# Performance work log

Hardware: AMD Instinct MI355X
Metric: run time of the kernel (lower is better)

Reference implementation:

```python
import jax, jax.numpy as jnp
import numpy as np

N = 50000   # vertices
E = 25000   # hyperedges
NNZ = 400000  # incidence pairs (v, e)
D_IN = 512
D_OUT = 512  # heads * out_channels, heads=1


def setup_inputs() -> dict:
    key = jax.random.key(0)
    kx, kw, kv, ke = jax.random.split(key, 4)
    X = jax.random.normal(kx, (N, D_IN), dtype=jnp.float32)
    W = jax.random.normal(kw, (D_OUT, D_IN), dtype=jnp.float32) * 0.02  # nn.Linear weight [out,in]
    vidx = jax.random.randint(kv, (NNZ,), 0, N, dtype=jnp.int32)
    eidx = jax.random.randint(ke, (NNZ,), 0, E, dtype=jnp.int32)
    # degE = 1/|e| (hyperedge size), degV = 1/deg(v), as precomputed by hyperg
    ones = jnp.ones((NNZ,), dtype=jnp.float32)
    edge_sz = jax.ops.segment_sum(ones, eidx, num_segments=E)
    vert_dg = jax.ops.segment_sum(ones, vidx, num_segments=N)
    degE = 1.0 / jnp.maximum(edge_sz, 1.0)
    degV = 1.0 / jnp.maximum(vert_dg, 1.0)
    Wdiag = jnp.ones((E,), dtype=jnp.float32)
    return {"X": X, "W": W, "degE": degE, "degV": degV, "Wdiag": Wdiag,
            "vidx": vidx, "eidx": eidx}


def reference(X, W, degE, degV, Wdiag, vidx, eidx):
    # Dense projection: X @ W^T (nn.Linear, no bias)
    Xp = jnp.einsum('nd,od->no', X, W)                      # [N, D_OUT]
    # Stage 1: vertex -> hyperedge (first_aggr: mean via degE), weighted by Wdiag
    Xe = jax.ops.segment_sum(Xp[vidx], eidx, num_segments=E)  # [E, D_OUT]
    Xe = Xe * (degE * Wdiag)[:, None]
    # Stage 2: hyperedge -> vertex, normalized by degV
    Xv = jax.ops.segment_sum(Xe[eidx], vidx, num_segments=N)  # [N, D_OUT]
    Xv = Xv * degV[:, None]
    return Xv
```

## Files before the change

kernel.cpp:

```cpp
#include <hip/hip_runtime.h>

typedef unsigned short u16;
typedef unsigned int   u32;
typedef __attribute__((ext_vector_type(4))) float f32x4;
typedef __attribute__((ext_vector_type(4))) u32   u32x4;
typedef __attribute__((ext_vector_type(8))) __bf16 bf16x8;

constexpr int NV   = 50000;
constexpr int NE   = 25000;
constexpr int NNZp = 400000;
constexpr int D    = 512;
constexpr int MP   = 50048;
constexpr int NBE  = 25;
constexpr int NBV  = 49;

static __device__ __forceinline__ u16 f2bf(float f) {
  u32 u = __float_as_uint(f);
  u32 r = (u + 0x7fffu + ((u >> 16) & 1u)) >> 16;
  return (u16)r;
}
static __device__ __forceinline__ u32 pk2(float a, float b) {
  return (u32)f2bf(a) | ((u32)f2bf(b) << 16);
}

static __device__ __forceinline__ void gload_lds16(const u16* g, u16* l) {
  __builtin_amdgcn_global_load_lds(
      (const __attribute__((address_space(1))) u32*)g,
      (__attribute__((address_space(3))) u32*)l, 16, 0, 0);
}

__global__ void zero_kernel(int* cntE, int* cntV) {
  int i = blockIdx.x * 256 + threadIdx.x;
  if (i < NE) cntE[i] = 0;
  if (i < NV) cntV[i] = 0;
}

__global__ void hist_kernel(const int* __restrict__ vidx, const int* __restrict__ eidx,
                            int* cntE, int* cntV) {
  int i = blockIdx.x * 256 + threadIdx.x;
  if (i < NNZp) {
    atomicAdd(&cntE[eidx[i]], 1);
    atomicAdd(&cntV[vidx[i]], 1);
  }
}

__global__ __launch_bounds__(256) void scan1_kernel(
    const int* __restrict__ cntE, const int* __restrict__ cntV,
    int* offE, int* offV, int* blkSum) {
  const bool isE = blockIdx.x < NBE;
  const int* cnt = isE ? cntE : cntV;
  int* off = isE ? offE : offV;
  const int len = isE ? NE : NV;
  const int t = threadIdx.x;
  const int base = (isE ? blockIdx.x : blockIdx.x - NBE) * 1024 + t * 4;
  int4 c = {0, 0, 0, 0};
  if (base + 4 <= len) c = *(const int4*)(cnt + base);
  else {
    if (base + 0 < len) c.x = cnt[base + 0];
    if (base + 1 < len) c.y = cnt[base + 1];
    if (base + 2 < len) c.z = cnt[base + 2];
    if (base + 3 < len) c.w = cnt[base + 3];
  }
  int s = c.x + c.y + c.z + c.w;
  __shared__ int sm[256];
  sm[t] = s;
  __syncthreads();
  for (int d = 1; d < 256; d <<= 1) {
    int u = (t >= d) ? sm[t - d] : 0;
    __syncthreads();
    sm[t] += u;
    __syncthreads();
  }
  int ex = sm[t] - s;
  int4 o;
  o.x = ex; o.y = o.x + c.x; o.z = o.y + c.y; o.w = o.z + c.z;
  if (base + 4 <= len) *(int4*)(off + base) = o;
  else {
    if (base + 0 < len) off[base + 0] = o.x;
    if (base + 1 < len) off[base + 1] = o.y;
    if (base + 2 < len) off[base + 2] = o.z;
    if (base + 3 < len) off[base + 3] = o.w;
  }
  if (t == 255) blkSum[blockIdx.x] = sm[255];
}

__global__ void scan2_kernel(int* blkSum) {
  int wv = threadIdx.x >> 6, lane = threadIdx.x & 63;
  int off = wv ? NBE : 0, len = wv ? NBV : NBE;
  int v = (lane < len) ? blkSum[off + lane] : 0;
  int incl = v;
#pragma unroll
  for (int d = 1; d < 64; d <<= 1) {
    int u = __shfl_up(incl, d, 64);
    if (lane >= d) incl += u;
  }
  if (lane < len) blkSum[off + lane] = incl - v;
}

__global__ __launch_bounds__(256) void scan3_kernel(
    int* offE, int* offV, int* curE, int* curV, const int* __restrict__ blkSum) {
  const bool isE = blockIdx.x < NBE;
  int* off = isE ? offE : offV;
  int* cur = isE ? curE : curV;
  const int len = isE ? NE : NV;
  const int pref = blkSum[blockIdx.x];
  const int base = (isE ? blockIdx.x : blockIdx.x - NBE) * 1024 + threadIdx.x * 4;
  if (base + 4 <= len) {
    int4 o = *(int4*)(off + base);
    o.x += pref; o.y += pref; o.z += pref; o.w += pref;
    *(int4*)(off + base) = o;
    *(int4*)(cur + base) = o;
  } else {
    for (int q = 0; q < 4; q++)
      if (base + q < len) { int v = off[base + q] + pref; off[base + q] = v; cur[base + q] = v; }
  }
}

__global__ void scatter_kernel(const int* __restrict__ vidx, const int* __restrict__ eidx,
                               int* curE, int* curV, int* csr_ev, int* csr_ve) {
  int i = blockIdx.x * 256 + threadIdx.x;
  if (i < NNZp) {
    int e = eidx[i], v = vidx[i];
    csr_ev[atomicAdd(&curE[e], 1)] = v;
    csr_ve[atomicAdd(&curV[v], 1)] = e;
  }
}

__global__ __launch_bounds__(256) void convert_kernel(
    const float* __restrict__ X, const float* __restrict__ W,
    u16* __restrict__ Xb, u16* __restrict__ Wb) {
  constexpr size_t NX = (size_t)NV * D;
  size_t i = ((size_t)blockIdx.x * 256 + threadIdx.x) * 8;
  const float* src;
  u16* dst;
  if (i < NX) { src = X + i; dst = Xb + i; }
  else        { src = W + (i - NX); dst = Wb + (i - NX); }
  f32x4 a = *(const f32x4*)src;
  f32x4 b = *(const f32x4*)(src + 4);
  u32x4 p = { pk2(a[0], a[1]), pk2(a[2], a[3]), pk2(b[0], b[1]), pk2(b[2], b[3]) };
  *(u32x4*)dst = p;
}

__global__ __launch_bounds__(256) void gemm_kernel(const u16* __restrict__ A,
                                                   const u16* __restrict__ B,
                                                   u16* __restrict__ C) {
  __shared__ u16 sA[128 * 32];
  __shared__ u16 sB[128 * 32];
  const int tid  = threadIdx.x;
  const int lane = tid & 63;
  const int wave = tid >> 6;
  const int bm = blockIdx.y * 128;
  const int bn = blockIdx.x * 128;
  const int wm = (wave >> 1) * 64;
  const int wn = (wave & 1) * 64;
  const int lr = lane & 15;
  const int lk = (lane >> 4) * 8;
  const int srow = lane >> 2;
  const int scol = (lane & 3) * 8;

  f32x4 acc[4][4] = {};

  for (int kt = 0; kt < D; kt += 32) {
    __syncthreads();
#pragma unroll
    for (int c = 0; c < 2; c++) {
      const int ar = wave * 16 + c * 64;
      gload_lds16(A + (size_t)(bm + ar + srow) * D + kt + scol, &sA[ar * 32]);
      gload_lds16(B + (size_t)(bn + ar + srow) * D + kt + scol, &sB[ar * 32]);
    }
    __syncthreads();

    bf16x8 af[4], bfr[4];
#pragma unroll
    for (int i = 0; i < 4; i++) af[i]  = *(const bf16x8*)&sA[(wm + i * 16 + lr) * 32 + lk];
#pragma unroll
    for (int j = 0; j < 4; j++) bfr[j] = *(const bf16x8*)&sB[(wn + j * 16 + lr) * 32 + lk];
#pragma unroll
    for (int i = 0; i < 4; i++)
#pragma unroll
      for (int j = 0; j < 4; j++)
        acc[i][j] = __builtin_amdgcn_mfma_f32_16x16x32_bf16(af[i], bfr[j], acc[i][j], 0, 0, 0);
  }

#pragma unroll
  for (int i = 0; i < 4; i++)
#pragma unroll
    for (int r = 0; r < 4; r++) {
      int row = bm + wm + i * 16 + (lane >> 4) * 4 + r;
      u16* crow = C + (size_t)row * D + bn + wn + lr;
#pragma unroll
      for (int j = 0; j < 4; j++) crow[j * 16] = f2bf(acc[i][j][r]);
    }
}

__global__ __launch_bounds__(256) void stage1_kernel(
    const u16* __restrict__ Xp, const int* __restrict__ offE, const int* __restrict__ cntE,
    const int* __restrict__ csr_ev, const float* __restrict__ degE,
    const float* __restrict__ Wdiag, u16* __restrict__ Xe) {
  const int lane = threadIdx.x & 63;
  const int e = blockIdx.x * 4 + (threadIdx.x >> 6);
  const int start = offE[e], cnt = cntE[e];
  float acc[8] = {};
  for (int base = 0; base < cnt; base += 64) {
    int n = min(64, cnt - base);
    int myidx = (base + lane < cnt) ? csr_ev[start + base + lane] : 0;
#pragma unroll 4
    for (int k = 0; k < n; k++) {
      int v = __shfl(myidx, k, 64);
      u32x4 p = *(const u32x4*)(Xp + (size_t)v * D + lane * 8);
#pragma unroll
      for (int q = 0; q < 4; q++) {
        u32 u = p[q];
        acc[2 * q]     += __uint_as_float(u << 16);
        acc[2 * q + 1] += __uint_as_float(u & 0xffff0000u);
      }
    }
  }
  float s = degE[e] * Wdiag[e];
  u32x4 o = { pk2(acc[0] * s, acc[1] * s), pk2(acc[2] * s, acc[3] * s),
              pk2(acc[4] * s, acc[5] * s), pk2(acc[6] * s, acc[7] * s) };
  *(u32x4*)(Xe + (size_t)e * D + lane * 8) = o;
}

__global__ __launch_bounds__(256) void stage2_kernel(
    const u16* __restrict__ Xe, const int* __restrict__ offV, const int* __restrict__ cntV,
    const int* __restrict__ csr_ve, const float* __restrict__ degV, float* __restrict__ out) {
  const int lane = threadIdx.x & 63;
  const int v = blockIdx.x * 4 + (threadIdx.x >> 6);
  const int start = offV[v], cnt = cntV[v];
  float acc[8] = {};
  for (int base = 0; base < cnt; base += 64) {
    int n = min(64, cnt - base);
    int myidx = (base + lane < cnt) ? csr_ve[start + base + lane] : 0;
#pragma unroll 4
    for (int k = 0; k < n; k++) {
      int e = __shfl(myidx, k, 64);
      u32x4 p = *(const u32x4*)(Xe + (size_t)e * D + lane * 8);
#pragma unroll
      for (int q = 0; q < 4; q++) {
        u32 u = p[q];
        acc[2 * q]     += __uint_as_float(u << 16);
        acc[2 * q + 1] += __uint_as_float(u & 0xffff0000u);
      }
    }
  }
  float s = degV[v];
  float* orow = out + (size_t)v * D + lane * 8;
  f32x4 o0 = { acc[0] * s, acc[1] * s, acc[2] * s, acc[3] * s };
  f32x4 o1 = { acc[4] * s, acc[5] * s, acc[6] * s, acc[7] * s };
  *(f32x4*)orow = o0;
  *(f32x4*)(orow + 4) = o1;
}

extern "C" void kernel_launch(void* const* d_in, const int* in_sizes, int n_in,
                              void* d_out, int out_size, void* d_ws, size_t ws_size,
                              hipStream_t stream) {
  const float* X     = (const float*)d_in[0];
  const float* W     = (const float*)d_in[1];
  const float* degE  = (const float*)d_in[2];
  const float* degV  = (const float*)d_in[3];
  const float* Wdiag = (const float*)d_in[4];
  const int*   vidx  = (const int*)d_in[5];
  const int*   eidx  = (const int*)d_in[6];
  float* out = (float*)d_out;

  char* p = (char*)d_ws;
  auto take = [&](size_t bytes) { char* r = p; p += (bytes + 255) & ~(size_t)255; return r; };
  u16* Xb     = (u16*)take((size_t)MP * D * 2);
  u16* Wb     = (u16*)take((size_t)D * D * 2);
  u16* Xp     = (u16*)take((size_t)MP * D * 2);
  u16* Xe     = (u16*)take((size_t)NE * D * 2);
  int* cntE   = (int*)take((size_t)NE * 4);
  int* offE   = (int*)take((size_t)NE * 4);
  int* curE   = (int*)take((size_t)NE * 4);
  int* cntV   = (int*)take((size_t)NV * 4);
  int* offV   = (int*)take((size_t)NV * 4);
  int* curV   = (int*)take((size_t)NV * 4);
  int* csr_ev = (int*)take((size_t)NNZp * 4);
  int* csr_ve = (int*)take((size_t)NNZp * 4);
  int* blkSum = (int*)take((size_t)(NBE + NBV) * 4);

  constexpr size_t NCONV = ((size_t)NV * D + (size_t)D * D) / 8 / 256;

  zero_kernel   <<<(NV + 255) / 256, 256, 0, stream>>>(cntE, cntV);
  hist_kernel   <<<(NNZp + 255) / 256, 256, 0, stream>>>(vidx, eidx, cntE, cntV);
  scan1_kernel  <<<NBE + NBV, 256, 0, stream>>>(cntE, cntV, offE, offV, blkSum);
  scan2_kernel  <<<1, 128, 0, stream>>>(blkSum);
  scan3_kernel  <<<NBE + NBV, 256, 0, stream>>>(offE, offV, curE, curV, blkSum);
  scatter_kernel<<<(NNZp + 255) / 256, 256, 0, stream>>>(vidx, eidx, curE, curV, csr_ev, csr_ve);
  convert_kernel<<<NCONV, 256, 0, stream>>>(X, W, Xb, Wb);
  gemm_kernel   <<<dim3(D / 128, MP / 128), 256, 0, stream>>>(Xb, Wb, Xp);
  stage1_kernel <<<NE / 4, 256, 0, stream>>>(Xp, offE, cntE, csr_ev, degE, Wdiag, Xe);
  stage2_kernel <<<NV / 4, 256, 0, stream>>>(Xe, offV, cntV, csr_ve, degV, out);
}
```

Before: 441.6 us.

## Split gather-reduce rows into column slices with 8 neighbors per wave in parallel

```diff
diff --git a/kernel.cpp b/kernel.cpp
--- a/kernel.cpp
+++ b/kernel.cpp
@@ -197,17 +197,20 @@
     const u16* __restrict__ Xp, const int* __restrict__ offE, const int* __restrict__ cntE,
     const int* __restrict__ csr_ev, const float* __restrict__ degE,
     const float* __restrict__ Wdiag, u16* __restrict__ Xe) {
-  const int lane = threadIdx.x & 63;
-  const int e = blockIdx.x * 4 + (threadIdx.x >> 6);
+  const int wave  = threadIdx.x >> 6;
+  const int lane  = threadIdx.x & 63;
+  const int g     = lane >> 3;
+  const int c     = lane & 7;
+  const int slice = blockIdx.x & 7;
+  const int e     = (blockIdx.x >> 3) * 4 + wave;
   const int start = offE[e], cnt = cntE[e];
+  const int col0  = slice * 64 + c * 8;
   float acc[8] = {};
-  for (int base = 0; base < cnt; base += 64) {
-    int n = min(64, cnt - base);
-    int myidx = (base + lane < cnt) ? csr_ev[start + base + lane] : 0;
-#pragma unroll 4
-    for (int k = 0; k < n; k++) {
-      int v = __shfl(myidx, k, 64);
-      u32x4 p = *(const u32x4*)(Xp + (size_t)v * D + lane * 8);
+  for (int base = 0; base < cnt; base += 8) {
+    int j = base + g;
+    if (j < cnt) {
+      int v = csr_ev[start + j];
+      u32x4 p = *(const u32x4*)(Xp + (size_t)v * D + col0);
 #pragma unroll
       for (int q = 0; q < 4; q++) {
         u32 u = p[q];
@@ -216,26 +219,39 @@
       }
     }
   }
-  float s = degE[e] * Wdiag[e];
-  u32x4 o = { pk2(acc[0] * s, acc[1] * s), pk2(acc[2] * s, acc[3] * s),
-              pk2(acc[4] * s, acc[5] * s), pk2(acc[6] * s, acc[7] * s) };
-  *(u32x4*)(Xe + (size_t)e * D + lane * 8) = o;
+#pragma unroll
+  for (int q = 0; q < 8; q++) {
+    float s = acc[q];
+    s += __shfl_xor(s, 8, 64);
+    s += __shfl_xor(s, 16, 64);
+    s += __shfl_xor(s, 32, 64);
+    acc[q] = s;
+  }
+  if (g == 0) {
+    float s = degE[e] * Wdiag[e];
+    u32x4 o = { pk2(acc[0] * s, acc[1] * s), pk2(acc[2] * s, acc[3] * s),
+                pk2(acc[4] * s, acc[5] * s), pk2(acc[6] * s, acc[7] * s) };
+    *(u32x4*)(Xe + (size_t)e * D + col0) = o;
+  }
 }
 
 __global__ __launch_bounds__(256) void stage2_kernel(
     const u16* __restrict__ Xe, const int* __restrict__ offV, const int* __restrict__ cntV,
     const int* __restrict__ csr_ve, const float* __restrict__ degV, float* __restrict__ out) {
-  const int lane = threadIdx.x & 63;
-  const int v = blockIdx.x * 4 + (threadIdx.x >> 6);
+  const int wave  = threadIdx.x >> 6;
+  const int lane  = threadIdx.x & 63;
+  const int g     = lane >> 3;
+  const int c     = lane & 7;
+  const int slice = blockIdx.x & 7;
+  const int v     = (blockIdx.x >> 3) * 4 + wave;
   const int start = offV[v], cnt = cntV[v];
+  const int col0  = slice * 64 + c * 8;
   float acc[8] = {};
-  for (int base = 0; base < cnt; base += 64) {
-    int n = min(64, cnt - base);
-    int myidx = (base + lane < cnt) ? csr_ve[start + base + lane] : 0;
-#pragma unroll 4
-    for (int k = 0; k < n; k++) {
-      int e = __shfl(myidx, k, 64);
-      u32x4 p = *(const u32x4*)(Xe + (size_t)e * D + lane * 8);
+  for (int base = 0; base < cnt; base += 8) {
+    int j = base + g;
+    if (j < cnt) {
+      int e = csr_ve[start + j];
+      u32x4 p = *(const u32x4*)(Xe + (size_t)e * D + col0);
 #pragma unroll
       for (int q = 0; q < 4; q++) {
         u32 u = p[q];
@@ -244,12 +260,22 @@
       }
     }
   }
-  float s = degV[v];
-  float* orow = out + (size_t)v * D + lane * 8;
-  f32x4 o0 = { acc[0] * s, acc[1] * s, acc[2] * s, acc[3] * s };
-  f32x4 o1 = { acc[4] * s, acc[5] * s, acc[6] * s, acc[7] * s };
-  *(f32x4*)orow = o0;
-  *(f32x4*)(orow + 4) = o1;
+#pragma unroll
+  for (int q = 0; q < 8; q++) {
+    float s = acc[q];
+    s += __shfl_xor(s, 8, 64);
+    s += __shfl_xor(s, 16, 64);
+    s += __shfl_xor(s, 32, 64);
+    acc[q] = s;
+  }
+  if (g == 0) {
+    float s = degV[v];
+    float* orow = out + (size_t)v * D + col0;
+    f32x4 o0 = { acc[0] * s, acc[1] * s, acc[2] * s, acc[3] * s };
+    f32x4 o1 = { acc[4] * s, acc[5] * s, acc[6] * s, acc[7] * s };
+    *(f32x4*)orow = o0;
+    *(f32x4*)(orow + 4) = o1;
+  }
 }
 
 extern "C" void kernel_launch(void* const* d_in, const int* in_sizes, int n_in,
@@ -290,6 +316,6 @@
   scatter_kernel<<<(NNZp + 255) / 256, 256, 0, stream>>>(vidx, eidx, curE, curV, csr_ev, csr_ve);
   convert_kernel<<<NCONV, 256, 0, stream>>>(X, W, Xb, Wb);
   gemm_kernel   <<<dim3(D / 128, MP / 128), 256, 0, stream>>>(Xb, Wb, Xp);
-  stage1_kernel <<<NE / 4, 256, 0, stream>>>(Xp, offE, cntE, csr_ev, degE, Wdiag, Xe);
-  stage2_kernel <<<NV / 4, 256, 0, stream>>>(Xe, offV, cntV, csr_ve, degV, out);
-}
+  stage1_kernel <<<(NE / 4) * 8, 256, 0, stream>>>(Xp, offE, cntE, csr_ev, degE, Wdiag, Xe);
+  stage2_kernel <<<(NV / 4) * 8, 256, 0, stream>>>(Xe, offV, cntV, csr_ve, degV, out);
+}
```

New measurement: 538.9 us. 22.1% more time.

## Split gather-aggregation columns into XCD-mapped slices for L2 locality

Applied to the files above, without the earlier changes.

```diff
diff --git a/kernel.cpp b/kernel.cpp
--- a/kernel.cpp
+++ b/kernel.cpp
@@ -13,6 +13,8 @@
 constexpr int MP   = 50048;
 constexpr int NBE  = 25;
 constexpr int NBV  = 49;
+constexpr int SG1  = 391;
+constexpr int SG2  = 1563;
 
 static __device__ __forceinline__ u16 f2bf(float f) {
   u32 u = __float_as_uint(f);
@@ -197,59 +199,75 @@
     const u16* __restrict__ Xp, const int* __restrict__ offE, const int* __restrict__ cntE,
     const int* __restrict__ csr_ev, const float* __restrict__ degE,
     const float* __restrict__ Wdiag, u16* __restrict__ Xe) {
+  const int wave = threadIdx.x >> 6;
   const int lane = threadIdx.x & 63;
-  const int e = blockIdx.x * 4 + (threadIdx.x >> 6);
-  const int start = offE[e], cnt = cntE[e];
+  const int g    = lane >> 2;
+  const int c    = lane & 3;
+  const int bid  = blockIdx.x;
+  const int xcd  = bid & 7;
+  const int tmp  = bid >> 3;
+  const int phase = (tmp >= SG1) ? 1 : 0;
+  const int sg    = tmp - phase * SG1;
+  const int slice = xcd + 8 * phase;
+  const int e     = sg * 64 + wave * 16 + g;
+  const int col0  = slice * 32 + c * 8;
+  int start = 0, cnt = 0;
+  if (e < NE) { start = offE[e]; cnt = cntE[e]; }
   float acc[8] = {};
-  for (int base = 0; base < cnt; base += 64) {
-    int n = min(64, cnt - base);
-    int myidx = (base + lane < cnt) ? csr_ev[start + base + lane] : 0;
-#pragma unroll 4
-    for (int k = 0; k < n; k++) {
-      int v = __shfl(myidx, k, 64);
-      u32x4 p = *(const u32x4*)(Xp + (size_t)v * D + lane * 8);
-#pragma unroll
-      for (int q = 0; q < 4; q++) {
-        u32 u = p[q];
-        acc[2 * q]     += __uint_as_float(u << 16);
-        acc[2 * q + 1] += __uint_as_float(u & 0xffff0000u);
-      }
+  int nxt = (cnt > 0) ? csr_ev[start] : 0;
+  for (int j = 0; j < cnt; j++) {
+    int v = nxt;
+    if (j + 1 < cnt) nxt = csr_ev[start + j + 1];
+    u32x4 p = *(const u32x4*)(Xp + (size_t)v * D + col0);
+#pragma unroll
+    for (int q = 0; q < 4; q++) {
+      u32 u = p[q];
+      acc[2 * q]     += __uint_as_float(u << 16);
+      acc[2 * q + 1] += __uint_as_float(u & 0xffff0000u);
     }
   }
-  float s = degE[e] * Wdiag[e];
-  u32x4 o = { pk2(acc[0] * s, acc[1] * s), pk2(acc[2] * s, acc[3] * s),
-              pk2(acc[4] * s, acc[5] * s), pk2(acc[6] * s, acc[7] * s) };
-  *(u32x4*)(Xe + (size_t)e * D + lane * 8) = o;
+  if (e < NE) {
+    float s = degE[e] * Wdiag[e];
+    u32x4 o = { pk2(acc[0] * s, acc[1] * s), pk2(acc[2] * s, acc[3] * s),
+                pk2(acc[4] * s, acc[5] * s), pk2(acc[6] * s, acc[7] * s) };
+    *(u32x4*)(Xe + (size_t)e * D + col0) = o;
+  }
 }
 
 __global__ __launch_bounds__(256) void stage2_kernel(
     const u16* __restrict__ Xe, const int* __restrict__ offV, const int* __restrict__ cntV,
     const int* __restrict__ csr_ve, const float* __restrict__ degV, float* __restrict__ out) {
+  const int wave = threadIdx.x >> 6;
   const int lane = threadIdx.x & 63;
-  const int v = blockIdx.x * 4 + (threadIdx.x >> 6);
-  const int start = offV[v], cnt = cntV[v];
+  const int g    = lane >> 3;
+  const int c    = lane & 7;
+  const int slice = blockIdx.x & 7;
+  const int sg    = blockIdx.x >> 3;
+  const int v     = sg * 32 + wave * 8 + g;
+  const int col0  = slice * 64 + c * 8;
+  int start = 0, cnt = 0;
+  if (v < NV) { start = offV[v]; cnt = cntV[v]; }
   float acc[8] = {};
-  for (int base = 0; base < cnt; base += 64) {
-    int n = min(64, cnt - base);
-    int myidx = (base + lane < cnt) ? csr_ve[start + base + lane] : 0;
-#pragma unroll 4
-    for (int k = 0; k < n; k++) {
-      int e = __shfl(myidx, k, 64);
-      u32x4 p = *(const u32x4*)(Xe + (size_t)e * D + lane * 8);
-#pragma unroll
-      for (int q = 0; q < 4; q++) {
-        u32 u = p[q];
-        acc[2 * q]     += __uint_as_float(u << 16);
-        acc[2 * q + 1] += __uint_as_float(u & 0xffff0000u);
-      }
+  int nxt = (cnt > 0) ? csr_ve[start] : 0;
+  for (int j = 0; j < cnt; j++) {
+    int e = nxt;
+    if (j + 1 < cnt) nxt = csr_ve[start + j + 1];
+    u32x4 p = *(const u32x4*)(Xe + (size_t)e * D + col0);
+#pragma unroll
+    for (int q = 0; q < 4; q++) {
+      u32 u = p[q];
+      acc[2 * q]     += __uint_as_float(u << 16);
+      acc[2 * q + 1] += __uint_as_float(u & 0xffff0000u);
     }
   }
-  float s = degV[v];
-  float* orow = out + (size_t)v * D + lane * 8;
-  f32x4 o0 = { acc[0] * s, acc[1] * s, acc[2] * s, acc[3] * s };
-  f32x4 o1 = { acc[4] * s, acc[5] * s, acc[6] * s, acc[7] * s };
-  *(f32x4*)orow = o0;
-  *(f32x4*)(orow + 4) = o1;
+  if (v < NV) {
+    float s = degV[v];
+    float* orow = out + (size_t)v * D + col0;
+    f32x4 o0 = { acc[0] * s, acc[1] * s, acc[2] * s, acc[3] * s };
+    f32x4 o1 = { acc[4] * s, acc[5] * s, acc[6] * s, acc[7] * s };
+    *(f32x4*)orow = o0;
+    *(f32x4*)(orow + 4) = o1;
+  }
 }
 
 extern "C" void kernel_launch(void* const* d_in, const int* in_sizes, int n_in,
@@ -290,6 +308,6 @@
   scatter_kernel<<<(NNZp + 255) / 256, 256, 0, stream>>>(vidx, eidx, curE, curV, csr_ev, csr_ve);
   convert_kernel<<<NCONV, 256, 0, stream>>>(X, W, Xb, Wb);
   gemm_kernel   <<<dim3(D / 128, MP / 128), 256, 0, stream>>>(Xb, Wb, Xp);
-  stage1_kernel <<<NE / 4, 256, 0, stream>>>(Xp, offE, cntE, csr_ev, degE, Wdiag, Xe);
-  stage2_kernel <<<NV / 4, 256, 0, stream>>>(Xe, offV, cntV, csr_ve, degV, out);
-}
+  stage1_kernel <<<SG1 * 16, 256, 0, stream>>>(Xp, offE, cntE, csr_ev, degE, Wdiag, Xe);
+  stage2_kernel <<<SG2 * 8, 256, 0, stream>>>(Xe, offV, cntV, csr_ve, degV, out);
+}
```

New measurement: 459.7 us. 1.04x slower.
